# Kernel optimization log

Hardware: AMD Instinct MI355X
Metric: run time of the kernel (lower is better)

The kernel has to match this reference:

```python
import jax, jax.numpy as jnp
import numpy as np

VOCAB = 32000
EMB = 200
HID = 128
B = 64
T = 64


def setup_inputs() -> dict:
    key = jax.random.key(0)
    ks = jax.random.split(key, 10)
    s = 0.05
    return {
        "tokens": jax.random.randint(ks[0], (B, T), 0, VOCAB, dtype=jnp.int32),
        "emb": jax.random.normal(ks[1], (VOCAB, EMB), jnp.float32) * s,
        "W0": jax.random.normal(ks[2], (EMB, 4 * HID), jnp.float32) * s,
        "U0": jax.random.normal(ks[3], (HID, 4 * HID), jnp.float32) * s,
        "b0": jax.random.normal(ks[4], (4 * HID,), jnp.float32) * s,
        "W1": jax.random.normal(ks[5], (HID, 4 * HID), jnp.float32) * s,
        "U1": jax.random.normal(ks[6], (HID, 4 * HID), jnp.float32) * s,
        "b1": jax.random.normal(ks[7], (4 * HID,), jnp.float32) * s,
        "Wout": jax.random.normal(ks[8], (HID, VOCAB), jnp.float32) * s,
        "bout": jax.random.normal(ks[9], (VOCAB,), jnp.float32) * s,
    }


def _lstm_cell(x, h, c, W, U, b):
    # Keras LSTMCell gate order: i, f, g(candidate), o
    z = x @ W + h @ U + b  # [B, 4H]
    i, f, g, o = jnp.split(z, 4, axis=-1)
    c_new = jax.nn.sigmoid(f) * c + jax.nn.sigmoid(i) * jnp.tanh(g)
    h_new = jax.nn.sigmoid(o) * jnp.tanh(c_new)
    return h_new, c_new


def reference(tokens, emb, W0, U0, b0, W1, U1, b1, Wout, bout):
    x = emb[tokens]                      # [B, T, EMB]
    xt = jnp.transpose(x, (1, 0, 2))     # time-major [T, B, EMB]
    zeros = jnp.zeros((tokens.shape[0], HID), x.dtype)
    init = (zeros, zeros, zeros, zeros)  # h0, c0, h1, c1

    def step(carry, xw):
        h0, c0, h1, c1 = carry
        h0, c0 = _lstm_cell(xw, h0, c0, W0, U0, b0)
        h1, c1 = _lstm_cell(h0, h1, c1, W1, U1, b1)
        out = jax.nn.relu(h1 @ Wout + bout)  # [B, VOCAB]
        return (h0, c0, h1, c1), out

    _, outs = jax.lax.scan(step, init, xt)   # [T, B, VOCAB]
    return jnp.transpose(outs, (1, 0, 2))    # [B, T, VOCAB]
```

## Files before the change

### kernel.cpp

```cpp
#include <hip/hip_runtime.h>
#include <stdint.h>
#include <stddef.h>

typedef _Float16 f16;
typedef _Float16 f16x2 __attribute__((ext_vector_type(2)));
typedef _Float16 f16x8 __attribute__((ext_vector_type(8)));
typedef float    f32x4 __attribute__((ext_vector_type(4)));

#define VOCAB 32000
#define EMBD  200
#define HID   128
#define NB    64
#define NT    64
#define G4    (4*HID)

__device__ __forceinline__ float sigf(float x) {
    return __builtin_amdgcn_rcpf(1.f + __expf(-x));
}
__device__ __forceinline__ float tanhf_(float x) {
    return 1.f - 2.f * __builtin_amdgcn_rcpf(1.f + __expf(2.f * x));
}

__global__ __launch_bounds__(256) void fused_prep(
    const int* __restrict__ tokens, const float* __restrict__ emb,
    const float* __restrict__ W0, const float* __restrict__ b0,
    const float* __restrict__ U0, const float* __restrict__ W1,
    const float* __restrict__ U1,
    float* __restrict__ z0, uint32_t* __restrict__ wp) {
    const int t = threadIdx.x;
    if (blockIdx.x >= 256) {
        int idx = (blockIdx.x - 256) * 256 + t;
        int m = idx >> 15;
        int rem = idx & 32767;
        int p = rem >> 9, j = rem & 511;
        const float* W = (m == 0) ? U0 : (m == 1) ? W1 : U1;
        f16x2 v;
        v[0] = (f16)W[(2 * p) * G4 + j];
        v[1] = (f16)W[(2 * p + 1) * G4 + j];
        ((f16x2*)wp)[idx] = v;
        return;
    }
    __shared__ __align__(16) float xs[EMBD * 16];
    __shared__ int tok[16];
    const int blk = blockIdx.x;
    if (t < 16) tok[t] = tokens[blk * 16 + t];
    __syncthreads();
    for (int i = t; i < EMBD * 16; i += 256) {
        int r = i / EMBD, k = i - r * EMBD;
        xs[k * 16 + r] = emb[(size_t)tok[r] * EMBD + k];
    }
    __syncthreads();
    const int j = t * 2;
    f32x4 accA[4], accB[4];
#pragma unroll
    for (int grp = 0; grp < 4; ++grp) {
        accA[grp] = f32x4{0.f, 0.f, 0.f, 0.f};
        accB[grp] = f32x4{0.f, 0.f, 0.f, 0.f};
    }
    for (int k = 0; k < EMBD; ++k) {
        float2 w = *(const float2*)(W0 + (size_t)k * G4 + j);
        const f32x4* xv = (const f32x4*)(xs + k * 16);
#pragma unroll
        for (int grp = 0; grp < 4; ++grp) {
            f32x4 x = xv[grp];
            accA[grp] += x * w.x;
            accB[grp] += x * w.y;
        }
    }
    float bx = b0[j], by = b0[j + 1];
#pragma unroll
    for (int grp = 0; grp < 4; ++grp)
#pragma unroll
        for (int r = 0; r < 4; ++r) {
            int row = blk * 16 + grp * 4 + r;
            float2 o; o.x = accA[grp][r] + bx; o.y = accB[grp][r] + by;
            *(float2*)(z0 + (size_t)row * G4 + j) = o;
        }
}

__global__ __launch_bounds__(512, 1) void scan_fused(
    const float* __restrict__ z0base, const uint32_t* __restrict__ wp,
    const float* __restrict__ b1, f16* __restrict__ H1,
    const float* __restrict__ Wout, f16* __restrict__ WoutT, int do_wt) {
    const int t = threadIdx.x;
    if (blockIdx.x >= 64) {
        if (!do_wt) return;
        __shared__ __align__(16) f16 tile[64 * 136];
        const int n0 = (blockIdx.x - 64) * 64;
        for (int i = t; i < 64 * 128; i += 512) {
            int k = i >> 6, n = i & 63;
            tile[n * 136 + k] = (f16)Wout[(size_t)k * VOCAB + n0 + n];
        }
        __syncthreads();
        for (int i = t; i < 1024; i += 512) {
            int n = i >> 4, u = i & 15;
            *(uint4*)(WoutT + (size_t)(n0 + n) * HID + u * 8) =
                *(const uint4*)&tile[n * 136 + u * 8];
        }
        return;
    }
    const int b = blockIdx.x;
    const int g = t >> 7, q = t & 127, jb = q << 2;
    __shared__ __align__(16) float zpart[4][G4];
    __shared__ __align__(16) f16 h0s[HID];
    __shared__ __align__(16) f16 h1s[HID];

    const f16x8* wp8 = (const f16x8*)wp;
    f16x2 wu0[64], ww1[64], wu1[64];
    const int wbase = (g * 16) * 128 + q;
#pragma unroll
    for (int kk = 0; kk < 16; ++kk) {
        *(f16x8*)&wu0[kk * 4] = wp8[0 * 8192 + wbase + kk * 128];
        *(f16x8*)&ww1[kk * 4] = wp8[1 * 8192 + wbase + kk * 128];
        *(f16x8*)&wu1[kk * 4] = wp8[2 * 8192 + wbase + kk * 128];
    }
    float b1a = 0.f, b1b = 0.f, b1c = 0.f, b1d = 0.f;
    if (t < HID) {
        b1a = b1[t]; b1b = b1[t + 128]; b1c = b1[t + 256]; b1d = b1[t + 384];
        h0s[t] = (f16)0.f; h1s[t] = (f16)0.f;
    }
    float c0 = 0.f, c1 = 0.f;
    __syncthreads();

    const float* zb = z0base + (size_t)b * NT * G4;
    f16* hout = H1 + (size_t)b * NT * HID;

    for (int step = 0; step < NT; ++step) {
        float za = 0.f, zbv = 0.f, zc = 0.f, zd = 0.f;
        if (t < HID) {
            const float* zr = zb + (size_t)step * G4 + t;
            za = zr[0]; zbv = zr[128]; zc = zr[256]; zd = zr[384];
        }
        float a0 = 0.f, a1 = 0.f, a2 = 0.f, a3 = 0.f;
        {
            f16x2 hh[16];
            const f16x8* hp = (const f16x8*)h0s + g * 4;
            *(f16x8*)&hh[0] = hp[0]; *(f16x8*)&hh[4] = hp[1];
            *(f16x8*)&hh[8] = hp[2]; *(f16x8*)&hh[12] = hp[3];
#pragma unroll
            for (int kk = 0; kk < 16; ++kk) {
                f16x2 h = hh[kk];
                a0 = __builtin_amdgcn_fdot2(wu0[kk * 4 + 0], h, a0, false);
                a1 = __builtin_amdgcn_fdot2(wu0[kk * 4 + 1], h, a1, false);
                a2 = __builtin_amdgcn_fdot2(wu0[kk * 4 + 2], h, a2, false);
                a3 = __builtin_amdgcn_fdot2(wu0[kk * 4 + 3], h, a3, false);
            }
        }
        *(f32x4*)&zpart[g][jb] = f32x4{a0, a1, a2, a3};
        __syncthreads();
        if (t < HID) {
            float zi = za  + zpart[0][t]       + zpart[1][t]       + zpart[2][t]       + zpart[3][t];
            float zf = zbv + zpart[0][t + 128] + zpart[1][t + 128] + zpart[2][t + 128] + zpart[3][t + 128];
            float zg = zc  + zpart[0][t + 256] + zpart[1][t + 256] + zpart[2][t + 256] + zpart[3][t + 256];
            float zo = zd  + zpart[0][t + 384] + zpart[1][t + 384] + zpart[2][t + 384] + zpart[3][t + 384];
            c0 = sigf(zf) * c0 + sigf(zi) * tanhf_(zg);
            h0s[t] = (f16)(sigf(zo) * tanhf_(c0));
        }
        __syncthreads();
        a0 = 0.f; a1 = 0.f; a2 = 0.f; a3 = 0.f;
        {
            f16x2 hh[16];
            const f16x8* hp0 = (const f16x8*)h0s + g * 4;
            *(f16x8*)&hh[0] = hp0[0]; *(f16x8*)&hh[4] = hp0[1];
            *(f16x8*)&hh[8] = hp0[2]; *(f16x8*)&hh[12] = hp0[3];
#pragma unroll
            for (int kk = 0; kk < 16; ++kk) {
                f16x2 h = hh[kk];
                a0 = __builtin_amdgcn_fdot2(ww1[kk * 4 + 0], h, a0, false);
                a1 = __builtin_amdgcn_fdot2(ww1[kk * 4 + 1], h, a1, false);
                a2 = __builtin_amdgcn_fdot2(ww1[kk * 4 + 2], h, a2, false);
                a3 = __builtin_amdgcn_fdot2(ww1[kk * 4 + 3], h, a3, false);
            }
            const f16x8* hp1 = (const f16x8*)h1s + g * 4;
            *(f16x8*)&hh[0] = hp1[0]; *(f16x8*)&hh[4] = hp1[1];
            *(f16x8*)&hh[8] = hp1[2]; *(f16x8*)&hh[12] = hp1[3];
#pragma unroll
            for (int kk = 0; kk < 16; ++kk) {
                f16x2 h = hh[kk];
                a0 = __builtin_amdgcn_fdot2(wu1[kk * 4 + 0], h, a0, false);
                a1 = __builtin_amdgcn_fdot2(wu1[kk * 4 + 1], h, a1, false);
                a2 = __builtin_amdgcn_fdot2(wu1[kk * 4 + 2], h, a2, false);
                a3 = __builtin_amdgcn_fdot2(wu1[kk * 4 + 3], h, a3, false);
            }
        }
        *(f32x4*)&zpart[g][jb] = f32x4{a0, a1, a2, a3};
        __syncthreads();
        if (t < HID) {
            float zi = b1a + zpart[0][t]       + zpart[1][t]       + zpart[2][t]       + zpart[3][t];
            float zf = b1b + zpart[0][t + 128] + zpart[1][t + 128] + zpart[2][t + 128] + zpart[3][t + 128];
            float zg = b1c + zpart[0][t + 256] + zpart[1][t + 256] + zpart[2][t + 256] + zpart[3][t + 256];
            float zo = b1d + zpart[0][t + 384] + zpart[1][t + 384] + zpart[2][t + 384] + zpart[3][t + 384];
            c1 = sigf(zf) * c1 + sigf(zi) * tanhf_(zg);
            float h1v = sigf(zo) * tanhf_(c1);
            h1s[t] = (f16)h1v;
            hout[step * HID + t] = (f16)h1v;
        }
        __syncthreads();
    }
}

__global__ __launch_bounds__(256) void prep_woutT(
    const float* __restrict__ Wout, f16* __restrict__ WoutT) {
    __shared__ __align__(16) f16 tile[64 * 136];
    const int n0 = blockIdx.x * 64;
    const int t = threadIdx.x;
    for (int i = t; i < 64 * 128; i += 256) {
        int k = i >> 6, n = i & 63;
        tile[n * 136 + k] = (f16)Wout[(size_t)k * VOCAB + n0 + n];
    }
    __syncthreads();
    for (int i = t; i < 1024; i += 256) {
        int n = i >> 4, u = i & 15;
        *(uint4*)(WoutT + (size_t)(n0 + n) * HID + u * 8) =
            *(const uint4*)&tile[n * 136 + u * 8];
    }
}

__global__ __launch_bounds__(256) void out_gemm(
    const f16* __restrict__ H1, const f16* __restrict__ WT,
    const float* __restrict__ bout, float* __restrict__ out) {
    __shared__ __align__(16) char lraw[128 * 132 * 4];
    f16* Asub = (f16*)lraw;
    f16* Bsub = (f16*)(lraw + 32768);
    const int m0 = blockIdx.x * 128;
    const int n0 = blockIdx.y * 128;
    const int t = threadIdx.x;

    const uint4* Ag = (const uint4*)(H1 + (size_t)m0 * HID);
    const uint4* Bg = (const uint4*)(WT + (size_t)n0 * HID);
#pragma unroll
    for (int i = 0; i < 8; ++i) {
        int Gr = i * 256 + t;
        int row = Gr >> 4, gg = Gr & 15;
        int d = (row << 4) | (gg ^ (row & 7));
        ((uint4*)Asub)[d] = Ag[Gr];
        ((uint4*)Bsub)[d] = Bg[Gr];
    }
    __syncthreads();

    const int w = t >> 6, l = t & 63;
    const int wm = (w >> 1) * 64, wn = (w & 1) * 64;
    const int lr = l & 15, lk = l >> 4;
    f32x4 zero = {0.f, 0.f, 0.f, 0.f};
    f32x4 acc[4][4];
#pragma unroll
    for (int mi = 0; mi < 4; ++mi)
#pragma unroll
        for (int ni = 0; ni < 4; ++ni) acc[mi][ni] = zero;

#pragma unroll
    for (int kc = 0; kc < 4; ++kc) {
        f16x8 af[4], bf[4];
#pragma unroll
        for (int mi = 0; mi < 4; ++mi) {
            int row = wm + mi * 16 + lr;
            int gg = kc * 4 + lk;
            af[mi] = *(const f16x8*)&Asub[(row << 7) + ((gg ^ (row & 7)) << 3)];
        }
#pragma unroll
        for (int ni = 0; ni < 4; ++ni) {
            int row = wn + ni * 16 + lr;
            int gg = kc * 4 + lk;
            bf[ni] = *(const f16x8*)&Bsub[(row << 7) + ((gg ^ (row & 7)) << 3)];
        }
#pragma unroll
        for (int mi = 0; mi < 4; ++mi)
#pragma unroll
            for (int ni = 0; ni < 4; ++ni)
                acc[mi][ni] = __builtin_amdgcn_mfma_f32_16x16x32_f16(
                    af[mi], bf[ni], acc[mi][ni], 0, 0, 0);
    }

    __syncthreads();
    float* ldsf = (float*)lraw;
#pragma unroll
    for (int mi = 0; mi < 4; ++mi) {
        int lrow = wm + mi * 16 + lk * 4;
#pragma unroll
        for (int ni = 0; ni < 4; ++ni) {
            int lcol = wn + ni * 16 + lr;
#pragma unroll
            for (int r = 0; r < 4; ++r)
                ldsf[(lrow + r) * 132 + lcol] = acc[mi][ni][r];
        }
    }
    __syncthreads();
    const int col = (t * 4) & 127;
    const int rbase = t >> 5;
    float4 bv = *(const float4*)&bout[n0 + col];
#pragma unroll
    for (int c = 0; c < 16; ++c) {
        int row = c * 8 + rbase;
        float4 v = *(const float4*)&ldsf[row * 132 + col];
        float4 o;
        o.x = v.x + bv.x; o.y = v.y + bv.y; o.z = v.z + bv.z; o.w = v.w + bv.w;
        o.x = o.x > 0.f ? o.x : 0.f;
        o.y = o.y > 0.f ? o.y : 0.f;
        o.z = o.z > 0.f ? o.z : 0.f;
        o.w = o.w > 0.f ? o.w : 0.f;
        *(float4*)&out[(size_t)(m0 + row) * VOCAB + n0 + col] = o;
    }
}

extern "C" void kernel_launch(void* const* d_in, const int* in_sizes, int n_in,
                              void* d_out, int out_size, void* d_ws, size_t ws_size,
                              hipStream_t stream) {
    const int*   tokens = (const int*)d_in[0];
    const float* emb  = (const float*)d_in[1];
    const float* W0   = (const float*)d_in[2];
    const float* U0   = (const float*)d_in[3];
    const float* b0   = (const float*)d_in[4];
    const float* W1   = (const float*)d_in[5];
    const float* U1   = (const float*)d_in[6];
    const float* b1   = (const float*)d_in[7];
    const float* Wout = (const float*)d_in[8];
    const float* bout = (const float*)d_in[9];
    float* out = (float*)d_out;

    char* ws = (char*)d_ws;
    float*    z0base = (float*)ws;
    uint32_t* wp     = (uint32_t*)(ws + 8388608);
    f16*      H1     = (f16*)(ws + 8781824);
    const bool big_ws = ws_size >= (size_t)18100000;
    f16*      WoutT  = big_ws ? (f16*)(ws + 9830400) : (f16*)ws;

    fused_prep<<<640, 256, 0, stream>>>(tokens, emb, W0, b0, U0, W1, U1, z0base, wp);
    scan_fused<<<564, 512, 0, stream>>>(z0base, wp, b1, H1, Wout, WoutT,
                                        big_ws ? 1 : 0);
    if (!big_ws)
        prep_woutT<<<500, 256, 0, stream>>>(Wout, WoutT);
    out_gemm<<<dim3(32, 250), 256, 0, stream>>>(H1, WoutT, bout, out);
}
```

Before: 274.4 us.

## Fuse scan, Wout transpose and output GEMM into one persistent flag-synchronized kernel

Merges the recurrent scan, the Wout transpose and the output GEMM into a single launch. GEMM blocks spin on per-timestep-pair flags, so output tiles for finished timesteps can run while the scan is still going. The scan is skewed so that layer 0 for step s+1 and layer 1 for step s run in the same phase, which cuts the barriers per step from four to two. H1 is now written time-major, and the GEMM uses 512-thread blocks with 128x128 tiles. This relies on scan blocks being scheduled before the spinning GEMM blocks, since lower block IDs are assumed to dispatch first, and it adds a memset plus atomic overhead.

```diff
diff --git a/kernel.cpp b/kernel.cpp
--- a/kernel.cpp
+++ b/kernel.cpp
@@ -78,15 +78,126 @@
         }
 }
 
-__global__ __launch_bounds__(512, 1) void scan_fused(
+__global__ __launch_bounds__(512, 1) void mega(
     const float* __restrict__ z0base, const uint32_t* __restrict__ wp,
     const float* __restrict__ b1, f16* __restrict__ H1,
-    const float* __restrict__ Wout, f16* __restrict__ WoutT, int do_wt) {
+    const float* __restrict__ Wout, f16* __restrict__ WoutT,
+    const float* __restrict__ bout, float* __restrict__ out,
+    uint32_t* __restrict__ flags, int role_ofs, int do_wait) {
+    __shared__ __align__(16) char smem[69632];
+    const int bid = blockIdx.x + role_ofs;
     const int t = threadIdx.x;
-    if (blockIdx.x >= 64) {
-        if (!do_wt) return;
-        __shared__ __align__(16) f16 tile[64 * 136];
-        const int n0 = (blockIdx.x - 64) * 64;
+
+    if (bid < 64) {
+        const int b = bid;
+        const int g = t >> 7, q = t & 127;
+        float* zA = (float*)smem;
+        float* zC = (float*)(smem + 8192);
+        f16* h0s = (f16*)(smem + 16384);
+        f16* h1s = (f16*)(smem + 16640);
+
+        const f16x8* wp8 = (const f16x8*)wp;
+        f16x2 wu0[64], ww1[64], wu1[64];
+        const int wbase = (g * 16) * 128 + q;
+#pragma unroll
+        for (int kk = 0; kk < 16; ++kk) {
+            *(f16x8*)&wu0[kk * 4] = wp8[0 * 8192 + wbase + kk * 128];
+            *(f16x8*)&ww1[kk * 4] = wp8[1 * 8192 + wbase + kk * 128];
+            *(f16x8*)&wu1[kk * 4] = wp8[2 * 8192 + wbase + kk * 128];
+        }
+        float b1a = 0.f, b1b = 0.f, b1c = 0.f, b1d = 0.f;
+        float c0 = 0.f, c1 = 0.f;
+        if (t < HID) {
+            b1a = b1[t]; b1b = b1[t + 128]; b1c = b1[t + 256]; b1d = b1[t + 384];
+            const float* zr = z0base + (size_t)b * NT * G4 + t;
+            float zi = zr[0], zf = zr[128], zg = zr[256], zo = zr[384];
+            (void)zf;
+            c0 = sigf(zi) * tanhf_(zg);
+            h0s[t] = (f16)(sigf(zo) * tanhf_(c0));
+            h1s[t] = (f16)0.f;
+        }
+        __syncthreads();
+
+        const float* zb = z0base + (size_t)b * NT * G4;
+
+        for (int s = 0; s < NT; ++s) {
+            float za = 0.f, zbv = 0.f, zc = 0.f, zd = 0.f;
+            if (t < HID) {
+                int nx = (s < 63) ? (s + 1) : 63;
+                const float* zr = zb + (size_t)nx * G4 + t;
+                za = zr[0]; zbv = zr[128]; zc = zr[256]; zd = zr[384];
+            }
+            float aA0 = 0.f, aA1 = 0.f, aA2 = 0.f, aA3 = 0.f;
+            float aC0 = 0.f, aC1 = 0.f, aC2 = 0.f, aC3 = 0.f;
+            {
+                f16x2 hh[16];
+                const f16x8* hp0 = (const f16x8*)h0s + g * 4;
+                *(f16x8*)&hh[0] = hp0[0]; *(f16x8*)&hh[4] = hp0[1];
+                *(f16x8*)&hh[8] = hp0[2]; *(f16x8*)&hh[12] = hp0[3];
+#pragma unroll
+                for (int kk = 0; kk < 16; ++kk) {
+                    f16x2 h = hh[kk];
+                    aA0 = __builtin_amdgcn_fdot2(wu0[kk * 4 + 0], h, aA0, false);
+                    aA1 = __builtin_amdgcn_fdot2(wu0[kk * 4 + 1], h, aA1, false);
+                    aA2 = __builtin_amdgcn_fdot2(wu0[kk * 4 + 2], h, aA2, false);
+                    aA3 = __builtin_amdgcn_fdot2(wu0[kk * 4 + 3], h, aA3, false);
+                    aC0 = __builtin_amdgcn_fdot2(ww1[kk * 4 + 0], h, aC0, false);
+                    aC1 = __builtin_amdgcn_fdot2(ww1[kk * 4 + 1], h, aC1, false);
+                    aC2 = __builtin_amdgcn_fdot2(ww1[kk * 4 + 2], h, aC2, false);
+                    aC3 = __builtin_amdgcn_fdot2(ww1[kk * 4 + 3], h, aC3, false);
+                }
+                const f16x8* hp1 = (const f16x8*)h1s + g * 4;
+                *(f16x8*)&hh[0] = hp1[0]; *(f16x8*)&hh[4] = hp1[1];
+                *(f16x8*)&hh[8] = hp1[2]; *(f16x8*)&hh[12] = hp1[3];
+#pragma unroll
+                for (int kk = 0; kk < 16; ++kk) {
+                    f16x2 h = hh[kk];
+                    aC0 = __builtin_amdgcn_fdot2(wu1[kk * 4 + 0], h, aC0, false);
+                    aC1 = __builtin_amdgcn_fdot2(wu1[kk * 4 + 1], h, aC1, false);
+                    aC2 = __builtin_amdgcn_fdot2(wu1[kk * 4 + 2], h, aC2, false);
+                    aC3 = __builtin_amdgcn_fdot2(wu1[kk * 4 + 3], h, aC3, false);
+                }
+            }
+            *(f32x4*)&zA[g * 512 + (q << 2)] = f32x4{aA0, aA1, aA2, aA3};
+            *(f32x4*)&zC[g * 512 + (q << 2)] = f32x4{aC0, aC1, aC2, aC3};
+            __syncthreads();
+            if (t < HID) {
+                float z1i = b1a + zC[t]        + zC[512 + t]        + zC[1024 + t]        + zC[1536 + t];
+                float z1f = b1b + zC[t + 128]  + zC[512 + t + 128]  + zC[1024 + t + 128]  + zC[1536 + t + 128];
+                float z1g = b1c + zC[t + 256]  + zC[512 + t + 256]  + zC[1024 + t + 256]  + zC[1536 + t + 256];
+                float z1o = b1d + zC[t + 384]  + zC[512 + t + 384]  + zC[1024 + t + 384]  + zC[1536 + t + 384];
+                c1 = sigf(z1f) * c1 + sigf(z1i) * tanhf_(z1g);
+                float h1v = sigf(z1o) * tanhf_(c1);
+                f16 hf = (f16)h1v;
+                h1s[t] = hf;
+                unsigned short hb = *(unsigned short*)&hf;
+                unsigned int partner = (unsigned int)__shfl_xor((int)hb, 1, 64) & 0xffffu;
+                if (!(t & 1)) {
+                    unsigned int packed = (unsigned int)hb | (partner << 16);
+                    unsigned int* row32 = (unsigned int*)(H1 + ((size_t)s * NB + b) * HID);
+                    __hip_atomic_store(row32 + (t >> 1), packed,
+                                       __ATOMIC_RELAXED, __HIP_MEMORY_SCOPE_AGENT);
+                }
+                if (s < 63) {
+                    float z0i = za  + zA[t]       + zA[512 + t]       + zA[1024 + t]       + zA[1536 + t];
+                    float z0f = zbv + zA[t + 128] + zA[512 + t + 128] + zA[1024 + t + 128] + zA[1536 + t + 128];
+                    float z0g = zc  + zA[t + 256] + zA[512 + t + 256] + zA[1024 + t + 256] + zA[1536 + t + 256];
+                    float z0o = zd  + zA[t + 384] + zA[512 + t + 384] + zA[1024 + t + 384] + zA[1536 + t + 384];
+                    c0 = sigf(z0f) * c0 + sigf(z0i) * tanhf_(z0g);
+                    h0s[t] = (f16)(sigf(z0o) * tanhf_(c0));
+                }
+            }
+            __syncthreads();
+            if (do_wait && (s & 1) && t == 0)
+                __hip_atomic_fetch_add(&flags[s >> 1], 1u,
+                                       __ATOMIC_RELEASE, __HIP_MEMORY_SCOPE_AGENT);
+        }
+        return;
+    }
+
+    if (bid < 564) {
+        f16* tile = (f16*)smem;
+        const int n0 = (bid - 64) * 64;
         for (int i = t; i < 64 * 128; i += 512) {
             int k = i >> 6, n = i & 63;
             tile[n * 136 + k] = (f16)Wout[(size_t)k * VOCAB + n0 + n];
@@ -97,208 +208,105 @@
             *(uint4*)(WoutT + (size_t)(n0 + n) * HID + u * 8) =
                 *(const uint4*)&tile[n * 136 + u * 8];
         }
+        if (do_wait) {
+            __syncthreads();
+            if (t == 0)
+                __hip_atomic_fetch_add(&flags[32], 1u,
+                                       __ATOMIC_RELEASE, __HIP_MEMORY_SCOPE_AGENT);
+        }
         return;
     }
-    const int b = blockIdx.x;
-    const int g = t >> 7, q = t & 127, jb = q << 2;
-    __shared__ __align__(16) float zpart[4][G4];
-    __shared__ __align__(16) f16 h0s[HID];
-    __shared__ __align__(16) f16 h1s[HID];
-
-    const f16x8* wp8 = (const f16x8*)wp;
-    f16x2 wu0[64], ww1[64], wu1[64];
-    const int wbase = (g * 16) * 128 + q;
-#pragma unroll
-    for (int kk = 0; kk < 16; ++kk) {
-        *(f16x8*)&wu0[kk * 4] = wp8[0 * 8192 + wbase + kk * 128];
-        *(f16x8*)&ww1[kk * 4] = wp8[1 * 8192 + wbase + kk * 128];
-        *(f16x8*)&wu1[kk * 4] = wp8[2 * 8192 + wbase + kk * 128];
-    }
-    float b1a = 0.f, b1b = 0.f, b1c = 0.f, b1d = 0.f;
-    if (t < HID) {
-        b1a = b1[t]; b1b = b1[t + 128]; b1c = b1[t + 256]; b1d = b1[t + 384];
-        h0s[t] = (f16)0.f; h1s[t] = (f16)0.f;
-    }
-    float c0 = 0.f, c1 = 0.f;
-    __syncthreads();
-
-    const float* zb = z0base + (size_t)b * NT * G4;
-    f16* hout = H1 + (size_t)b * NT * HID;
-
-    for (int step = 0; step < NT; ++step) {
-        float za = 0.f, zbv = 0.f, zc = 0.f, zd = 0.f;
-        if (t < HID) {
-            const float* zr = zb + (size_t)step * G4 + t;
-            za = zr[0]; zbv = zr[128]; zc = zr[256]; zd = zr[384];
-        }
-        float a0 = 0.f, a1 = 0.f, a2 = 0.f, a3 = 0.f;
-        {
-            f16x2 hh[16];
-            const f16x8* hp = (const f16x8*)h0s + g * 4;
-            *(f16x8*)&hh[0] = hp[0]; *(f16x8*)&hh[4] = hp[1];
-            *(f16x8*)&hh[8] = hp[2]; *(f16x8*)&hh[12] = hp[3];
-#pragma unroll
-            for (int kk = 0; kk < 16; ++kk) {
-                f16x2 h = hh[kk];
-                a0 = __builtin_amdgcn_fdot2(wu0[kk * 4 + 0], h, a0, false);
-                a1 = __builtin_amdgcn_fdot2(wu0[kk * 4 + 1], h, a1, false);
-                a2 = __builtin_amdgcn_fdot2(wu0[kk * 4 + 2], h, a2, false);
-                a3 = __builtin_amdgcn_fdot2(wu0[kk * 4 + 3], h, a3, false);
-            }
-        }
-        *(f32x4*)&zpart[g][jb] = f32x4{a0, a1, a2, a3};
-        __syncthreads();
-        if (t < HID) {
-            float zi = za  + zpart[0][t]       + zpart[1][t]       + zpart[2][t]       + zpart[3][t];
-            float zf = zbv + zpart[0][t + 128] + zpart[1][t + 128] + zpart[2][t + 128] + zpart[3][t + 128];
-            float zg = zc  + zpart[0][t + 256] + zpart[1][t + 256] + zpart[2][t + 256] + zpart[3][t + 256];
-            float zo = zd  + zpart[0][t + 384] + zpart[1][t + 384] + zpart[2][t + 384] + zpart[3][t + 384];
-            c0 = sigf(zf) * c0 + sigf(zi) * tanhf_(zg);
-            h0s[t] = (f16)(sigf(zo) * tanhf_(c0));
-        }
-        __syncthreads();
-        a0 = 0.f; a1 = 0.f; a2 = 0.f; a3 = 0.f;
-        {
-            f16x2 hh[16];
-            const f16x8* hp0 = (const f16x8*)h0s + g * 4;
-            *(f16x8*)&hh[0] = hp0[0]; *(f16x8*)&hh[4] = hp0[1];
-            *(f16x8*)&hh[8] = hp0[2]; *(f16x8*)&hh[12] = hp0[3];
-#pragma unroll
-            for (int kk = 0; kk < 16; ++kk) {
-                f16x2 h = hh[kk];
-                a0 = __builtin_amdgcn_fdot2(ww1[kk * 4 + 0], h, a0, false);
-                a1 = __builtin_amdgcn_fdot2(ww1[kk * 4 + 1], h, a1, false);
-                a2 = __builtin_amdgcn_fdot2(ww1[kk * 4 + 2], h, a2, false);
-                a3 = __builtin_amdgcn_fdot2(ww1[kk * 4 + 3], h, a3, false);
-            }
-            const f16x8* hp1 = (const f16x8*)h1s + g * 4;
-            *(f16x8*)&hh[0] = hp1[0]; *(f16x8*)&hh[4] = hp1[1];
-            *(f16x8*)&hh[8] = hp1[2]; *(f16x8*)&hh[12] = hp1[3];
-#pragma unroll
-            for (int kk = 0; kk < 16; ++kk) {
-                f16x2 h = hh[kk];
-                a0 = __builtin_amdgcn_fdot2(wu1[kk * 4 + 0], h, a0, false);
-                a1 = __builtin_amdgcn_fdot2(wu1[kk * 4 + 1], h, a1, false);
-                a2 = __builtin_amdgcn_fdot2(wu1[kk * 4 + 2], h, a2, false);
-                a3 = __builtin_amdgcn_fdot2(wu1[kk * 4 + 3], h, a3, false);
-            }
-        }
-        *(f32x4*)&zpart[g][jb] = f32x4{a0, a1, a2, a3};
-        __syncthreads();
-        if (t < HID) {
-            float zi = b1a + zpart[0][t]       + zpart[1][t]       + zpart[2][t]       + zpart[3][t];
-            float zf = b1b + zpart[0][t + 128] + zpart[1][t + 128] + zpart[2][t + 128] + zpart[3][t + 128];
-            float zg = b1c + zpart[0][t + 256] + zpart[1][t + 256] + zpart[2][t + 256] + zpart[3][t + 256];
-            float zo = b1d + zpart[0][t + 384] + zpart[1][t + 384] + zpart[2][t + 384] + zpart[3][t + 384];
-            c1 = sigf(zf) * c1 + sigf(zi) * tanhf_(zg);
-            float h1v = sigf(zo) * tanhf_(c1);
-            h1s[t] = (f16)h1v;
-            hout[step * HID + t] = (f16)h1v;
-        }
-        __syncthreads();
-    }
-}
-
-__global__ __launch_bounds__(256) void prep_woutT(
-    const float* __restrict__ Wout, f16* __restrict__ WoutT) {
-    __shared__ __align__(16) f16 tile[64 * 136];
-    const int n0 = blockIdx.x * 64;
-    const int t = threadIdx.x;
-    for (int i = t; i < 64 * 128; i += 256) {
-        int k = i >> 6, n = i & 63;
-        tile[n * 136 + k] = (f16)Wout[(size_t)k * VOCAB + n0 + n];
-    }
-    __syncthreads();
-    for (int i = t; i < 1024; i += 256) {
-        int n = i >> 4, u = i & 15;
-        *(uint4*)(WoutT + (size_t)(n0 + n) * HID + u * 8) =
-            *(const uint4*)&tile[n * 136 + u * 8];
-    }
-}
-
-__global__ __launch_bounds__(256) void out_gemm(
-    const f16* __restrict__ H1, const f16* __restrict__ WT,
-    const float* __restrict__ bout, float* __restrict__ out) {
-    __shared__ __align__(16) char lraw[128 * 132 * 4];
-    f16* Asub = (f16*)lraw;
-    f16* Bsub = (f16*)(lraw + 32768);
-    const int m0 = blockIdx.x * 128;
-    const int n0 = blockIdx.y * 128;
-    const int t = threadIdx.x;
-
-    const uint4* Ag = (const uint4*)(H1 + (size_t)m0 * HID);
-    const uint4* Bg = (const uint4*)(WT + (size_t)n0 * HID);
-#pragma unroll
-    for (int i = 0; i < 8; ++i) {
-        int Gr = i * 256 + t;
-        int row = Gr >> 4, gg = Gr & 15;
-        int d = (row << 4) | (gg ^ (row & 7));
-        ((uint4*)Asub)[d] = Ag[Gr];
-        ((uint4*)Bsub)[d] = Bg[Gr];
-    }
-    __syncthreads();
-
-    const int w = t >> 6, l = t & 63;
-    const int wm = (w >> 1) * 64, wn = (w & 1) * 64;
-    const int lr = l & 15, lk = l >> 4;
-    f32x4 zero = {0.f, 0.f, 0.f, 0.f};
-    f32x4 acc[4][4];
-#pragma unroll
-    for (int mi = 0; mi < 4; ++mi)
-#pragma unroll
-        for (int ni = 0; ni < 4; ++ni) acc[mi][ni] = zero;
-
-#pragma unroll
-    for (int kc = 0; kc < 4; ++kc) {
-        f16x8 af[4], bf[4];
+
+    {
+        const int gid = bid - 564;
+        const int j = gid / 250;
+        const int n = gid % 250;
+        if (do_wait) {
+            if (t == 0) {
+                while (__hip_atomic_load(&flags[32], __ATOMIC_ACQUIRE,
+                                         __HIP_MEMORY_SCOPE_AGENT) < 500u)
+                    __builtin_amdgcn_s_sleep(8);
+                while (__hip_atomic_load(&flags[j], __ATOMIC_ACQUIRE,
+                                         __HIP_MEMORY_SCOPE_AGENT) < 64u)
+                    __builtin_amdgcn_s_sleep(8);
+            }
+            __syncthreads();
+        }
+        f16* Asub = (f16*)smem;
+        f16* Bsub = (f16*)(smem + 32768);
+        const uint4* Ag = (const uint4*)(H1 + (size_t)(j * 128) * HID);
+        const uint4* Bg = (const uint4*)(WoutT + (size_t)(n * 128) * HID);
+#pragma unroll
+        for (int i = 0; i < 4; ++i) {
+            int Gr = i * 512 + t;
+            int row = Gr >> 4, gg = Gr & 15;
+            int d = (row << 4) | (gg ^ (row & 7));
+            ((uint4*)Asub)[d] = Ag[Gr];
+            ((uint4*)Bsub)[d] = Bg[Gr];
+        }
+        __syncthreads();
+
+        const int w = t >> 6, l = t & 63;
+        const int wm = (w >> 2) * 64, wn = (w & 3) * 32;
+        const int lr = l & 15, lk = l >> 4;
+        f32x4 acc[4][2];
+#pragma unroll
+        for (int mi = 0; mi < 4; ++mi)
+#pragma unroll
+            for (int ni = 0; ni < 2; ++ni) acc[mi][ni] = f32x4{0.f, 0.f, 0.f, 0.f};
+
+#pragma unroll
+        for (int kc = 0; kc < 4; ++kc) {
+            f16x8 af[4], bf[2];
+            int gg = kc * 4 + lk;
+#pragma unroll
+            for (int mi = 0; mi < 4; ++mi) {
+                int row = wm + mi * 16 + lr;
+                af[mi] = *(const f16x8*)&Asub[(row << 7) + ((gg ^ (row & 7)) << 3)];
+            }
+#pragma unroll
+            for (int ni = 0; ni < 2; ++ni) {
+                int row = wn + ni * 16 + lr;
+                bf[ni] = *(const f16x8*)&Bsub[(row << 7) + ((gg ^ (row & 7)) << 3)];
+            }
+#pragma unroll
+            for (int mi = 0; mi < 4; ++mi)
+#pragma unroll
+                for (int ni = 0; ni < 2; ++ni)
+                    acc[mi][ni] = __builtin_amdgcn_mfma_f32_16x16x32_f16(
+                        af[mi], bf[ni], acc[mi][ni], 0, 0, 0);
+        }
+
+        __syncthreads();
+        float* ldsf = (float*)smem;
 #pragma unroll
         for (int mi = 0; mi < 4; ++mi) {
-            int row = wm + mi * 16 + lr;
-            int gg = kc * 4 + lk;
-            af[mi] = *(const f16x8*)&Asub[(row << 7) + ((gg ^ (row & 7)) << 3)];
-        }
-#pragma unroll
-        for (int ni = 0; ni < 4; ++ni) {
-            int row = wn + ni * 16 + lr;
-            int gg = kc * 4 + lk;
-            bf[ni] = *(const f16x8*)&Bsub[(row << 7) + ((gg ^ (row & 7)) << 3)];
-        }
-#pragma unroll
-        for (int mi = 0; mi < 4; ++mi)
-#pragma unroll
-            for (int ni = 0; ni < 4; ++ni)
-                acc[mi][ni] = __builtin_amdgcn_mfma_f32_16x16x32_f16(
-                    af[mi], bf[ni], acc[mi][ni], 0, 0, 0);
-    }
-
-    __syncthreads();
-    float* ldsf = (float*)lraw;
-#pragma unroll
-    for (int mi = 0; mi < 4; ++mi) {
-        int lrow = wm + mi * 16 + lk * 4;
-#pragma unroll
-        for (int ni = 0; ni < 4; ++ni) {
-            int lcol = wn + ni * 16 + lr;
-#pragma unroll
-            for (int r = 0; r < 4; ++r)
-                ldsf[(lrow + r) * 132 + lcol] = acc[mi][ni][r];
-        }
-    }
-    __syncthreads();
-    const int col = (t * 4) & 127;
-    const int rbase = t >> 5;
-    float4 bv = *(const float4*)&bout[n0 + col];
-#pragma unroll
-    for (int c = 0; c < 16; ++c) {
-        int row = c * 8 + rbase;
-        float4 v = *(const float4*)&ldsf[row * 132 + col];
-        float4 o;
-        o.x = v.x + bv.x; o.y = v.y + bv.y; o.z = v.z + bv.z; o.w = v.w + bv.w;
-        o.x = o.x > 0.f ? o.x : 0.f;
-        o.y = o.y > 0.f ? o.y : 0.f;
-        o.z = o.z > 0.f ? o.z : 0.f;
-        o.w = o.w > 0.f ? o.w : 0.f;
-        *(float4*)&out[(size_t)(m0 + row) * VOCAB + n0 + col] = o;
+            int lrow = wm + mi * 16 + lk * 4;
+#pragma unroll
+            for (int ni = 0; ni < 2; ++ni) {
+                int lcol = wn + ni * 16 + lr;
+#pragma unroll
+                for (int r = 0; r < 4; ++r)
+                    ldsf[(lrow + r) * 132 + lcol] = acc[mi][ni][r];
+            }
+        }
+        __syncthreads();
+        const int col = (t & 31) * 4;
+        const int rb = t >> 5;
+        float4 bv = *(const float4*)&bout[n * 128 + col];
+#pragma unroll
+        for (int c = 0; c < 8; ++c) {
+            int row = c * 16 + rb;
+            float4 v = *(const float4*)&ldsf[row * 132 + col];
+            float4 o;
+            o.x = v.x + bv.x; o.y = v.y + bv.y; o.z = v.z + bv.z; o.w = v.w + bv.w;
+            o.x = o.x > 0.f ? o.x : 0.f;
+            o.y = o.y > 0.f ? o.y : 0.f;
+            o.z = o.z > 0.f ? o.z : 0.f;
+            o.w = o.w > 0.f ? o.w : 0.f;
+            int orow = (row & 63) * 64 + 2 * j + (row >> 6);
+            *(float4*)&out[(size_t)orow * VOCAB + n * 128 + col] = o;
+        }
     }
 }
 
@@ -321,13 +329,21 @@
     float*    z0base = (float*)ws;
     uint32_t* wp     = (uint32_t*)(ws + 8388608);
     f16*      H1     = (f16*)(ws + 8781824);
-    const bool big_ws = ws_size >= (size_t)18100000;
-    f16*      WoutT  = big_ws ? (f16*)(ws + 9830400) : (f16*)ws;
+    uint32_t* flags  = (uint32_t*)(ws + 9830400);
+    const bool big_ws = ws_size >= (size_t)18026496;
+    f16*      WoutT  = big_ws ? (f16*)(ws + 9834496) : (f16*)ws;
 
     fused_prep<<<640, 256, 0, stream>>>(tokens, emb, W0, b0, U0, W1, U1, z0base, wp);
-    scan_fused<<<564, 512, 0, stream>>>(z0base, wp, b1, H1, Wout, WoutT,
-                                        big_ws ? 1 : 0);
-    if (!big_ws)
-        prep_woutT<<<500, 256, 0, stream>>>(Wout, WoutT);
-    out_gemm<<<dim3(32, 250), 256, 0, stream>>>(H1, WoutT, bout, out);
-}
+    if (big_ws) {
+        hipMemsetAsync(flags, 0, 256, stream);
+        mega<<<8564, 512, 0, stream>>>(z0base, wp, b1, H1, Wout, WoutT, bout, out,
+                                       flags, 0, 1);
+    } else {
+        mega<<<64,   512, 0, stream>>>(z0base, wp, b1, H1, Wout, WoutT, bout, out,
+                                       flags, 0, 0);
+        mega<<<500,  512, 0, stream>>>(z0base, wp, b1, H1, Wout, WoutT, bout, out,
+                                       flags, 64, 0);
+        mega<<<8000, 512, 0, stream>>>(z0base, wp, b1, H1, Wout, WoutT, bout, out,
+                                       flags, 564, 0);
+    }
+}
```

Measured after the change: 448.8 us. 63.6% more time.
